# Kernel optimization log

Hardware: AMD Instinct MI355X
Metric: run time of the kernel (lower is better)

The kernel has to match this reference:

```python
import jax, jax.numpy as jnp
import numpy as np

L, H, P = 16384, 1024, 512
DT_MIN, DT_MAX = 1e-3, 1e-1
STEP_RESCALE = 1.0


def setup_inputs() -> dict:
    key = jax.random.key(0)
    ks = jax.random.split(key, 7)
    input_sequence = jax.random.normal(ks[0], (L, H), jnp.float32)
    # eigenvalues with negative real part (left half plane), HiPPO-like imag parts
    Lambda_re = -(jax.random.uniform(ks[1], (P,), jnp.float32) * 0.9 + 0.1)
    Lambda_im = jnp.pi * jnp.arange(P, dtype=jnp.float32)
    B = jax.random.normal(ks[2], (P, H, 2), jnp.float32) / jnp.sqrt(2.0 * H)   # real/imag of B_tilde (P,H)
    C = jax.random.normal(ks[3], (H, P, 2), jnp.float32) / jnp.sqrt(2.0 * P)   # real/imag of C_tilde (H,P)
    D = jax.random.normal(ks[4], (H,), jnp.float32)
    u01 = jax.random.uniform(ks[5], (P, 1), jnp.float32)
    log_step = jnp.log(DT_MIN) + u01 * (jnp.log(DT_MAX) - jnp.log(DT_MIN))     # (P,1)
    return dict(input_sequence=input_sequence, Lambda_re=Lambda_re, Lambda_im=Lambda_im,
                B=B, C=C, D=D, log_step=log_step)


def _binop(q_i, q_j):
    # diagonal linear recurrence composition: (A, b) pairs
    A_i, b_i = q_i
    A_j, b_j = q_j
    return A_j * A_i, A_j * b_i + b_j


def reference(input_sequence, Lambda_re, Lambda_im, B, C, D, log_step):
    Lambda = Lambda_re + 1j * Lambda_im                        # (P,) complex64
    B_tilde = B[..., 0] + 1j * B[..., 1]                       # (P,H)
    C_tilde = C[..., 0] + 1j * C[..., 1]                       # (H,P)
    step = STEP_RESCALE * jnp.exp(log_step[:, 0])              # (P,)
    # ZOH discretization
    Lambda_bar = jnp.exp(Lambda * step)                        # (P,)
    B_bar = ((Lambda_bar - 1.0) / Lambda)[:, None] * B_tilde   # (P,H)
    # Bu_elements: (L,P) complex
    Bu = input_sequence.astype(B_bar.dtype) @ B_bar.T
    Lambda_elems = jnp.broadcast_to(Lambda_bar, Bu.shape)      # (L,P)
    # parallel associative scan over the diagonal recurrence x_t = Lambda_bar*x_{t-1} + Bu_t
    _, xs = jax.lax.associative_scan(_binop, (Lambda_elems, Bu))
    ys = 2.0 * (xs @ C_tilde.T).real                           # conj_sym => factor 2, (L,H)
    return ys + D * input_sequence
```

## Files before the change

### kernel.cpp

```cpp
#include <hip/hip_runtime.h>
#include <math.h>

#define L_SEQ 16384
#define H_DIM 1024
#define P_DIM 512
#define N2P   1024
#define KDIM  1024
#define NTILE 32
#define CHUNK 64
#define NCHUNK 256

typedef __attribute__((ext_vector_type(8))) short short8;
typedef __attribute__((ext_vector_type(4))) float f32x4;

__device__ __forceinline__ unsigned short f2bf(float f){
    unsigned int u = __float_as_uint(f);
    u = (u + 0x7FFFu + ((u >> 16) & 1u)) >> 16;
    return (unsigned short)u;
}
__device__ __forceinline__ float bf2f(unsigned int lo16){
    return __uint_as_float(lo16 << 16);
}

__global__ void k_prep_lambda(const float* __restrict__ lre, const float* __restrict__ lim,
                              const float* __restrict__ lstep,
                              float* __restrict__ lam, float* __restrict__ coef,
                              float* __restrict__ lpow)
{
    int p = threadIdx.x;
    double step = exp((double)lstep[p]);
    double dr = (double)lre[p], di = (double)lim[p];
    double ar = dr*step, ai = di*step;
    double er = exp(ar);
    double lbr = er*cos(ai), lbi = er*sin(ai);
    lam[2*p] = (float)lbr; lam[2*p+1] = (float)lbi;
    double nr = lbr - 1.0, ni = lbi;
    double d2 = dr*dr + di*di;
    coef[2*p]   = (float)((nr*dr + ni*di)/d2);
    coef[2*p+1] = (float)((ni*dr - nr*di)/d2);
    double xr = lbr, xi = lbi;
    #pragma unroll
    for (int s=0;s<6;s++){ double t = xr*xr - xi*xi; xi = 2.0*xr*xi; xr = t; }
    lpow[2*p] = (float)xr; lpow[2*p+1] = (float)xi;
}

__global__ __launch_bounds__(256)
void k_prep_BB(const float* __restrict__ B, const float* __restrict__ coef,
               unsigned short* __restrict__ BB)
{
    int i = blockIdx.x*256 + threadIdx.x;
    int p = i >> 10, h = i & 1023;
    float br = B[2*i], bi = B[2*i+1];
    float cr = coef[2*p], ci = coef[2*p+1];
    BB[(size_t)(2*p)*H_DIM + h]   = f2bf(cr*br - ci*bi);
    BB[(size_t)(2*p+1)*H_DIM + h] = f2bf(cr*bi + ci*br);
}

__global__ __launch_bounds__(256)
void k_prep_CC(const float* __restrict__ C, unsigned short* __restrict__ CC)
{
    int i = blockIdx.x*256 + threadIdx.x;
    int h = i >> 9, p = i & 511;
    float cr = C[2*i], ci = C[2*i+1];
    CC[(size_t)h*N2P + 2*p]     = f2bf(2.f*cr);
    CC[(size_t)h*N2P + 2*p + 1] = f2bf(-2.f*ci);
}

__global__ __launch_bounds__(256)
void k_cast(const float4* __restrict__ u, unsigned short* __restrict__ o)
{
    int i = blockIdx.x*256 + threadIdx.x;
    float4 a = u[2*i], b = u[2*i+1];
    union { short8 v; unsigned short s[8]; } r;
    r.s[0]=f2bf(a.x); r.s[1]=f2bf(a.y); r.s[2]=f2bf(a.z); r.s[3]=f2bf(a.w);
    r.s[4]=f2bf(b.x); r.s[5]=f2bf(b.y); r.s[6]=f2bf(b.z); r.s[7]=f2bf(b.w);
    *reinterpret_cast<short8*>(o + (size_t)i*8) = r.v;
}

template<int EPI>
__global__ __launch_bounds__(512, 2)
void gemm256(const unsigned short* __restrict__ A, const unsigned short* __restrict__ Bm,
             float* __restrict__ Cf, unsigned short* __restrict__ Cb,
             const float* __restrict__ Dv, const unsigned short* __restrict__ U16)
{
    __shared__ char lds[131072];
    const int tid  = threadIdx.x;
    const int lane = tid & 63;
    const int wid  = tid >> 6;
    const int wm = wid >> 2, wn = wid & 3;
    const int wg = ((int)blockIdx.x & 7) * 32 + ((int)blockIdx.x >> 3);
    const int tm = wg >> 2, tn = wg & 3;
    const int lr = lane & 15;

    const int srow = wid*16 + (lane >> 2);
    const int scol = (((lane & 3) ^ ((lane >> 2) & 3)) << 3);
    const size_t aS0 = (size_t)(tm*256 + srow) * KDIM + scol;
    const size_t bS0 = (size_t)(tn*256 + srow) * KDIM + scol;
    const int ldsW = wid * 1024;

    const int kc   = (((lane >> 4) << 4) ^ ((lr & 3) << 4));
    const int aOff = (wm*128 + lr)*64 + kc;
    const int bOff = 65536 + (wn*64 + lr)*64 + kc;

#define GLOAD(SRC, DST) __builtin_amdgcn_global_load_lds( \
        (const __attribute__((address_space(1))) void*)(SRC), \
        (__attribute__((address_space(3))) void*)(DST), 16, 0, 0)
#define STAGE_A(tt) do{ int bb_ = ((tt)&3)*16384; \
    const unsigned short* s_ = A + aS0 + (size_t)(tt)*32; \
    GLOAD(s_,                    lds + bb_ + ldsW); \
    GLOAD(s_ + (size_t)128*KDIM, lds + bb_ + 8192 + ldsW); }while(0)
#define STAGE_B(tt) do{ int bb_ = 65536 + ((tt)&3)*16384; \
    const unsigned short* s_ = Bm + bS0 + (size_t)(tt)*32; \
    GLOAD(s_,                    lds + bb_ + ldsW); \
    GLOAD(s_ + (size_t)128*KDIM, lds + bb_ + 8192 + ldsW); }while(0)
#define RD(OFF) (*(const short8*)(lds + (OFF)))
#define MFMA(a,b,c) __builtin_amdgcn_mfma_f32_16x16x32_bf16(a,b,c,0,0,0)
#define BAR __builtin_amdgcn_s_barrier()

    short8 af[8], bfr[4];
    f32x4 acc[8][4];
    #pragma unroll
    for (int m=0;m<8;m++)
        #pragma unroll
        for (int n=0;n<4;n++) acc[m][n] = (f32x4){0.f,0.f,0.f,0.f};

    STAGE_A(0); STAGE_B(0); STAGE_A(1); STAGE_B(1); STAGE_A(2); STAGE_B(2);

    for (int t = 0; t < NTILE; ++t) {
        const int sb = (t & 3) * 16384;
        const int tt = (t+3 < NTILE) ? t+3 : NTILE-1;
        STAGE_A(tt);
        asm volatile("s_waitcnt vmcnt(10)" ::: "memory");
        BAR;
        #pragma unroll
        for (int m=0;m<8;m++) af[m] = RD(sb + aOff + m*1024);
        bfr[0] = RD(sb + bOff);
        bfr[1] = RD(sb + bOff + 1024);
        __builtin_amdgcn_s_setprio(1);
        #pragma unroll
        for (int m=0;m<8;m++){
            acc[m][0] = MFMA(af[m], bfr[0], acc[m][0]);
            acc[m][1] = MFMA(af[m], bfr[1], acc[m][1]);
        }
        __builtin_amdgcn_s_setprio(0);
        STAGE_B(tt);
        BAR;
        bfr[2] = RD(sb + bOff + 2048);
        bfr[3] = RD(sb + bOff + 3072);
        __builtin_amdgcn_s_setprio(1);
        #pragma unroll
        for (int m=0;m<8;m++){
            acc[m][2] = MFMA(af[m], bfr[2], acc[m][2]);
            acc[m][3] = MFMA(af[m], bfr[3], acc[m][3]);
        }
        __builtin_amdgcn_s_setprio(0);
    }
    asm volatile("s_waitcnt vmcnt(0)" ::: "memory");

    const int orow0 = tm*256 + wm*128 + (lane>>4)*4;
    const int ocol0 = tn*256 + wn*64 + lr;
    #pragma unroll
    for (int m=0;m<8;m++){
        #pragma unroll
        for (int n=0;n<4;n++){
            int row = orow0 + m*16, col = ocol0 + n*16;
            #pragma unroll
            for (int j=0;j<4;j++){
                size_t idx = (size_t)(row + j)*N2P + col;
                if (EPI) Cf[idx] = acc[m][n][j] + Dv[col]*bf2f(U16[idx]);
                else     Cb[idx] = f2bf(acc[m][n][j]);
            }
        }
    }
#undef GLOAD
#undef STAGE_A
#undef STAGE_B
#undef RD
#undef MFMA
#undef BAR
}

__global__ __launch_bounds__(512)
void k_agg(const unsigned int* __restrict__ Bu, const float* __restrict__ lam,
           float* __restrict__ agg)
{
    int p = threadIdx.x, c = blockIdx.x;
    float lrr = lam[2*p], lii = lam[2*p+1];
    float xr = 0.f, xi = 0.f;
    const unsigned int* b2 = Bu + (size_t)c*CHUNK*512 + p;
    #pragma unroll 4
    for (int t=0;t<CHUNK;t++){
        unsigned int b = b2[(size_t)t*512];
        float br = __uint_as_float(b << 16);
        float bi = __uint_as_float(b & 0xffff0000u);
        float tr = lrr*xr - lii*xi + br;
        xi = lrr*xi + lii*xr + bi;
        xr = tr;
    }
    agg[((size_t)c*P_DIM + p)*2]     = xr;
    agg[((size_t)c*P_DIM + p)*2 + 1] = xi;
}

__global__ __launch_bounds__(256)
void k_scan(const float* __restrict__ agg, const float* __restrict__ lpow,
            float* __restrict__ xinit)
{
    __shared__ float sr[NCHUNK], si[NCHUNK];
    int c = threadIdx.x, p = blockIdx.x;
    float xr = agg[((size_t)c*P_DIM + p)*2];
    float xi = agg[((size_t)c*P_DIM + p)*2 + 1];
    sr[c] = xr; si[c] = xi;
    float wr = lpow[2*p], wi = lpow[2*p+1];
    for (int s=1; s<NCHUNK; s<<=1){
        __syncthreads();
        float ur = 0.f, ui = 0.f;
        if (c >= s){ ur = sr[c-s]; ui = si[c-s]; }
        __syncthreads();
        xr += wr*ur - wi*ui;
        xi += wr*ui + wi*ur;
        sr[c] = xr; si[c] = xi;
        float t = wr*wr - wi*wi; wi = 2.f*wr*wi; wr = t;
    }
    __syncthreads();
    float er = 0.f, ei = 0.f;
    if (c > 0){ er = sr[c-1]; ei = si[c-1]; }
    xinit[((size_t)c*P_DIM + p)*2]     = er;
    xinit[((size_t)c*P_DIM + p)*2 + 1] = ei;
}

__global__ __launch_bounds__(512)
void k_apply(const unsigned int* __restrict__ Bu, const float* __restrict__ lam,
             const float* __restrict__ xinit, unsigned int* __restrict__ xs)
{
    int p = threadIdx.x, c = blockIdx.x;
    float lrr = lam[2*p], lii = lam[2*p+1];
    float xr = xinit[((size_t)c*P_DIM + p)*2];
    float xi = xinit[((size_t)c*P_DIM + p)*2 + 1];
    const unsigned int* b2 = Bu + (size_t)c*CHUNK*512 + p;
    unsigned int* o = xs + (size_t)c*CHUNK*512 + p;
    #pragma unroll 4
    for (int t=0;t<CHUNK;t++){
        unsigned int b = b2[(size_t)t*512];
        float br = __uint_as_float(b << 16);
        float bi = __uint_as_float(b & 0xffff0000u);
        float tr = lrr*xr - lii*xi + br;
        xi = lrr*xi + lii*xr + bi;
        xr = tr;
        o[(size_t)t*512] = (unsigned int)f2bf(xr) | ((unsigned int)f2bf(xi) << 16);
    }
}

extern "C" void kernel_launch(void* const* d_in, const int* in_sizes, int n_in,
                              void* d_out, int out_size, void* d_ws, size_t ws_size,
                              hipStream_t stream)
{
    const float* u   = (const float*)d_in[0];
    const float* lre = (const float*)d_in[1];
    const float* lim = (const float*)d_in[2];
    const float* B   = (const float*)d_in[3];
    const float* C   = (const float*)d_in[4];
    const float* D   = (const float*)d_in[5];
    const float* ls  = (const float*)d_in[6];
    float* out = (float*)d_out;

    char* w = (char*)d_ws;
    unsigned short* u16  = (unsigned short*)(w + 0);
    unsigned short* xs16 = (unsigned short*)(w + 33554432);
    unsigned short* Bu16 = (unsigned short*)(w + 67108864);
    unsigned short* BB   = (unsigned short*)(w + 100663296);
    unsigned short* CC   = (unsigned short*)(w + 102760448);
    float* lam   = (float*)(w + 104857600);
    float* coef  = (float*)(w + 104861696);
    float* lpow  = (float*)(w + 104865792);
    float* agg   = (float*)(w + 104869888);
    float* xinit = (float*)(w + 105918464);

    k_prep_lambda<<<1, P_DIM, 0, stream>>>(lre, lim, ls, lam, coef, lpow);
    k_prep_BB<<<(P_DIM*H_DIM)/256, 256, 0, stream>>>(B, coef, BB);
    k_prep_CC<<<(H_DIM*P_DIM)/256, 256, 0, stream>>>(C, CC);
    k_cast<<<(L_SEQ*H_DIM)/(256*8), 256, 0, stream>>>((const float4*)u, u16);

    gemm256<0><<<256, 512, 0, stream>>>(u16, BB, nullptr, Bu16, nullptr, nullptr);

    k_agg<<<NCHUNK, P_DIM, 0, stream>>>((const unsigned int*)Bu16, lam, agg);
    k_scan<<<P_DIM, NCHUNK, 0, stream>>>(agg, lpow, xinit);
    k_apply<<<NCHUNK, P_DIM, 0, stream>>>((const unsigned int*)Bu16, lam, xinit,
                                          (unsigned int*)xs16);

    gemm256<1><<<256, 512, 0, stream>>>(xs16, CC, out, nullptr, D, u16);
}
```

Before: 135.9 us.

## Restructure GEMM main loop with single-phase LDS reads and new swizzle

Issues both A and B global-to-LDS stages at the top of each k-iteration. All fragments are then read with inline-asm ds_read_b128 using immediate offsets and one lgkmcnt wait, followed by all 32 MFMAs in one block. The LDS XOR swizzle pattern changes to reduce bank conflicts. The two half-phases with a barrier between them are replaced by a single phase with a trailing barrier. This cuts address arithmetic and barrier overhead, but removes the overlap of B loads with the first MFMA half and relies on the manual vmcnt and swizzle values being correct.

Result: no change. 136.8 us (+0.7%).

```diff
diff --git a/kernel.cpp b/kernel.cpp
--- a/kernel.cpp
+++ b/kernel.cpp
@@ -12,6 +12,7 @@
 
 typedef __attribute__((ext_vector_type(8))) short short8;
 typedef __attribute__((ext_vector_type(4))) float f32x4;
+typedef __attribute__((address_space(3))) const char* lds3_t;
 
 __device__ __forceinline__ unsigned short f2bf(float f){
     unsigned int u = __float_as_uint(f);
@@ -93,14 +94,14 @@
     const int lr = lane & 15;
 
     const int srow = wid*16 + (lane >> 2);
-    const int scol = (((lane & 3) ^ ((lane >> 2) & 3)) << 3);
+    const int scol = (((lane & 3) ^ ((lane >> 3) & 3)) << 3);
     const size_t aS0 = (size_t)(tm*256 + srow) * KDIM + scol;
     const size_t bS0 = (size_t)(tn*256 + srow) * KDIM + scol;
     const int ldsW = wid * 1024;
 
-    const int kc   = (((lane >> 4) << 4) ^ ((lr & 3) << 4));
+    const int kc   = (((lane >> 4) ^ ((lr >> 1) & 3)) << 4);
     const int aOff = (wm*128 + lr)*64 + kc;
-    const int bOff = 65536 + (wn*64 + lr)*64 + kc;
+    const int bOff = (wn*64  + lr)*64 + kc;
 
 #define GLOAD(SRC, DST) __builtin_amdgcn_global_load_lds( \
         (const __attribute__((address_space(1))) void*)(SRC), \
@@ -113,7 +114,7 @@
     const unsigned short* s_ = Bm + bS0 + (size_t)(tt)*32; \
     GLOAD(s_,                    lds + bb_ + ldsW); \
     GLOAD(s_ + (size_t)128*KDIM, lds + bb_ + 8192 + ldsW); }while(0)
-#define RD(OFF) (*(const short8*)(lds + (OFF)))
+#define DSR(D, P, IMM) asm volatile("ds_read_b128 %0, %1 offset:" IMM : "=v"(D) : "v"(P))
 #define MFMA(a,b,c) __builtin_amdgcn_mfma_f32_16x16x32_bf16(a,b,c,0,0,0)
 #define BAR __builtin_amdgcn_s_barrier()
 
@@ -128,32 +129,31 @@
 
     for (int t = 0; t < NTILE; ++t) {
         const int sb = (t & 3) * 16384;
-        const int tt = (t+3 < NTILE) ? t+3 : NTILE-1;
+        const int tt = (t < NTILE-3) ? t+3 : NTILE-1;
         STAGE_A(tt);
-        asm volatile("s_waitcnt vmcnt(10)" ::: "memory");
+        STAGE_B(tt);
+        asm volatile("s_waitcnt vmcnt(12)" ::: "memory");
         BAR;
-        #pragma unroll
-        for (int m=0;m<8;m++) af[m] = RD(sb + aOff + m*1024);
-        bfr[0] = RD(sb + bOff);
-        bfr[1] = RD(sb + bOff + 1024);
+        lds3_t pa = (lds3_t)(lds + sb + aOff);
+        lds3_t pb = (lds3_t)(lds + 65536 + sb + bOff);
+        DSR(af[0], pa, "0");    DSR(af[1], pa, "1024");
+        DSR(af[2], pa, "2048"); DSR(af[3], pa, "3072");
+        DSR(af[4], pa, "4096"); DSR(af[5], pa, "5120");
+        DSR(af[6], pa, "6144"); DSR(af[7], pa, "7168");
+        DSR(bfr[0], pb, "0");    DSR(bfr[1], pb, "1024");
+        DSR(bfr[2], pb, "2048"); DSR(bfr[3], pb, "3072");
+        asm volatile("s_waitcnt lgkmcnt(0)" ::: "memory");
+        __builtin_amdgcn_sched_barrier(0);
         __builtin_amdgcn_s_setprio(1);
         #pragma unroll
         for (int m=0;m<8;m++){
             acc[m][0] = MFMA(af[m], bfr[0], acc[m][0]);
             acc[m][1] = MFMA(af[m], bfr[1], acc[m][1]);
-        }
-        __builtin_amdgcn_s_setprio(0);
-        STAGE_B(tt);
-        BAR;
-        bfr[2] = RD(sb + bOff + 2048);
-        bfr[3] = RD(sb + bOff + 3072);
-        __builtin_amdgcn_s_setprio(1);
-        #pragma unroll
-        for (int m=0;m<8;m++){
             acc[m][2] = MFMA(af[m], bfr[2], acc[m][2]);
             acc[m][3] = MFMA(af[m], bfr[3], acc[m][3]);
         }
         __builtin_amdgcn_s_setprio(0);
+        BAR;
     }
     asm volatile("s_waitcnt vmcnt(0)" ::: "memory");
 
@@ -175,7 +175,7 @@
 #undef GLOAD
 #undef STAGE_A
 #undef STAGE_B
-#undef RD
+#undef DSR
 #undef MFMA
 #undef BAR
 }
```
